# Kernel optimization log

Measured on AMD Instinct MI355X. Metric: run time of the kernel, lower is better.

Reference implementation:

```python
import jax, jax.numpy as jnp
import numpy as np

NSUB = 2          # fixed RK4 substeps per output interval (deterministic stand-in for adaptive dopri5)
SLOPE = 1.0 / 5.5  # leaky_relu negative slope used by g and OutputNN


def setup_inputs() -> dict:
    key = jax.random.key(0)
    ks = iter(jax.random.split(key, 40))
    B, Tp, Tf = 256, 32, 256
    D, H, HF, HG, HO = 1, 100, 275, 75, 75

    def rn(shape, s=0.05):
        return jax.random.normal(next(ks), shape, jnp.float32) * s

    # past: [B, Tp, 1+D] with strictly increasing times in column 0
    past_t = jnp.sort(jax.random.uniform(next(ks), (B, Tp), jnp.float32) * Tp, axis=1)
    past_x = jax.random.normal(next(ks), (B, Tp, D), jnp.float32)
    past = jnp.concatenate([past_t[:, :, None], past_x], axis=2)
    # future times start after the last past time, strictly increasing
    t_future = past_t[:, -1:] + jnp.sort(
        jax.random.uniform(next(ks), (B, Tf), jnp.float32) * 0.1 * Tf, axis=1)

    return dict(
        past=past,
        h0=jnp.zeros((B, H), jnp.float32),
        t_future=t_future,
        eps=jax.random.normal(next(ks), (H, B), jnp.float32),
        fW1=rn((HF, H + 1)), fb1=rn((HF,)), fW2=rn((HF, HF)), fb2=rn((HF,)),
        fW3=rn((H, HF)), fb3=rn((H,)),
        gru_Wih=rn((3 * H, D)), gru_Whh=rn((3 * H, H)),
        gru_bih=rn((3 * H,)), gru_bhh=rn((3 * H,)),
        gW1=rn((HG, H)), gb1=rn((HG,)), gW2=rn((HG, HG)), gb2=rn((HG,)),
        gW3=rn((2, HG)), gb3=rn((2,)),
        oW1=rn((HO, H)), ob1=rn((HO,)), oW2=rn((HO, HO)), ob2=rn((HO,)),
        oW3=rn((D, HO)), ob3=rn((D,)),
    )


def _leaky(x):
    return jnp.where(x >= 0, x, SLOPE * x)


def reference(past, h0, t_future, eps,
              fW1, fb1, fW2, fb2, fW3, fb3,
              gru_Wih, gru_Whh, gru_bih, gru_bhh,
              gW1, gb1, gW2, gb2, gW3, gb3,
              oW1, ob1, oW2, ob2, oW3, ob3):
    def field(t, y):  # t: [B], y: [B, H] -> dy/dt: [B, H]  (f module)
        x = jnp.concatenate([t[:, None], y], axis=1)
        x = jnp.tanh(x @ fW1.T + fb1)
        x = jnp.tanh(x @ fW2.T + fb2)
        return jnp.tanh(x @ fW3.T + fb3)

    def integrate(y0, t0, t1):  # batched fixed-step RK4 from t0 to t1 (per-batch times)
        dt = ((t1 - t0) / NSUB)[:, None]  # [B, 1]
        dts = dt[:, 0]
        def body(y, i):
            t = t0 + i * dts
            k1 = field(t, y)
            k2 = field(t + 0.5 * dts, y + 0.5 * dt * k1)
            k3 = field(t + 0.5 * dts, y + 0.5 * dt * k2)
            k4 = field(t + dts, y + dt * k3)
            return y + dt * (k1 + 2.0 * k2 + 2.0 * k3 + k4) / 6.0, None
        y, _ = jax.lax.scan(body, y0, jnp.arange(NSUB, dtype=y0.dtype))
        return y

    def gru(x, h):  # torch.nn.GRUCell math
        gi = x @ gru_Wih.T + gru_bih
        gh = h @ gru_Whh.T + gru_bhh
        ir, iz, inn = jnp.split(gi, 3, axis=1)
        hr, hz, hn = jnp.split(gh, 3, axis=1)
        r = jax.nn.sigmoid(ir + hr)
        z = jax.nn.sigmoid(iz + hz)
        n = jnp.tanh(inn + r * hn)
        return (1.0 - z) * n + z * h

    times = past[:, :, 0]   # [B, Tp]
    data = past[:, :, 1:]   # [B, Tp, D]

    # first GRUODE step: evolve h0 from t0-1 to t0, then GRU update with x0
    h = gru(data[:, 0], integrate(h0, times[:, 0] - 1.0, times[:, 0]))
    xs = (jnp.swapaxes(data[:, 1:], 0, 1), times[:, :-1].T, times[:, 1:].T)
    def pbody(hc, s):
        x, tp, tc = s
        return gru(x, integrate(hc, tp, tc)), None
    h, _ = jax.lax.scan(pbody, h, xs)

    # g head -> (loc, |scale|), reproducing the concat/view of the original
    gx = _leaky(h @ gW1.T + gb1)
    gx = _leaky(gx @ gW2.T + gb2)
    gx = gx @ gW3.T + gb3                                   # [B, 2]
    pr = jnp.concatenate([gx[:, 0], jnp.abs(gx[:, 1])]).reshape(-1, 2)
    loc, scale = pr[:, 0], pr[:, 1]                          # [B], [B]

    # Sampler: Normal(loc, scale).rsample([H]) reparameterized with eps [H, B]
    z0 = (loc[None, :] + scale[None, :] * eps).T             # [B, H]

    # integrate z0 across future time grid
    def fbody(y, s):
        tp, tc = s
        yn = integrate(y, tp, tc)
        return yn, yn
    _, traj = jax.lax.scan(fbody, z0, (t_future[:, :-1].T, t_future[:, 1:].T))
    out = jnp.swapaxes(jnp.concatenate([z0[None], traj], axis=0), 0, 1)  # [B, Tf, H]

    # OutputNN head
    o = _leaky(out @ oW1.T + ob1)
    o = _leaky(o @ oW2.T + ob2)
    return o @ oW3.T + ob3  # [B, Tf, D]
```

## Files before the change

### kernel.cpp

```cpp
#include <hip/hip_runtime.h>
#include <hip/hip_fp16.h>

typedef _Float16 f16;
typedef _Float16 f16x2 __attribute__((ext_vector_type(2)));
typedef _Float16 f16x8 __attribute__((ext_vector_type(8)));
typedef float f32x4 __attribute__((ext_vector_type(4)));
typedef unsigned short u16;
typedef unsigned int u32;

__device__ __forceinline__ float fdot2v(f16x2 a, f16x2 b, float c){
#if __has_builtin(__builtin_amdgcn_fdot2)
  return __builtin_amdgcn_fdot2(a, b, c, false);
#else
  return c + (float)a.x * (float)b.x + (float)a.y * (float)b.y;
#endif
}

__device__ __forceinline__ float rcp_f(float x){
#if __has_builtin(__builtin_amdgcn_rcpf)
  return __builtin_amdgcn_rcpf(x);
#else
  return 1.f / x;
#endif
}

__device__ __forceinline__ float tanh_f(float x){
  return 1.f - 2.f * rcp_f(__expf(2.f * x) + 1.f);
}
__device__ __forceinline__ float sigm_f(float x){
  return rcp_f(1.f + __expf(-x));
}
__device__ __forceinline__ float leaky_f(float x){
  return x >= 0.f ? x : x * (1.0f / 5.5f);
}

template<int NP>
__device__ __forceinline__ void ld_pairs(const float* W, int row, int ncols, int c0,
                                         f16x2* dst, bool valid){
  const float* base = W + (long)row * ncols;
#pragma unroll
  for (int p = 0; p < NP; p++){
    int c = c0 + 2 * p;
    f16x2 v;
    v.x = (valid && c     < ncols) ? (f16)base[c]     : (f16)0.f;
    v.y = (valid && c + 1 < ncols) ? (f16)base[c + 1] : (f16)0.f;
    dst[p] = v;
  }
}

template<int NCH>
__device__ __forceinline__ float dot_chunks(const f16x2* w, const f16x8* x, int chunk0){
  float a0 = 0.f, a1 = 0.f, a2 = 0.f, a3 = 0.f;
#pragma unroll
  for (int c = 0; c < NCH; c++){
    union { f16x8 v; f16x2 h[4]; } u;
    u.v = x[chunk0 + c];
    a0 = fdot2v(w[4*c + 0], u.h[0], a0);
    a1 = fdot2v(w[4*c + 1], u.h[1], a1);
    a2 = fdot2v(w[4*c + 2], u.h[2], a2);
    a3 = fdot2v(w[4*c + 3], u.h[3], a3);
  }
  return (a0 + a1) + (a2 + a3);
}

__device__ __forceinline__ f16x8 ldfrag(const float* W, int row, int ncols, int k0, bool valid){
  f16x8 v;
#pragma unroll
  for (int j = 0; j < 8; j++){
    int c = k0 + j;
    v[j] = (valid && c < ncols) ? (f16)W[(long)row * ncols + c] : (f16)0.f;
  }
  return v;
}

__device__ __forceinline__ float sel4(f32x4 a, int c){
  float v = a.x;
  v = (c == 1) ? a.y : v;
  v = (c == 2) ? a.z : v;
  v = (c == 3) ? a.w : v;
  return v;
}

#define MFMA16(A,B,C) __builtin_amdgcn_mfma_f32_16x16x32_f16((A),(B),(C),0,0,0)

struct FRM {
  f16x8 a1[2][4];
  f16x8 a2[2][9];
  f16x8 af[13];
  f16x2 w3b[9];
  float w1tw, b1w, b2w;
  float b3w;
};

struct DEC {
  f16x2 dW1[16]; f16x2 dW2[12]; f16x2 dW3;
  float ob1v, ob2v, ob3v;
};

__device__ __forceinline__ void load_field_mfma(FRM& R, int tid,
    const float* fW1, const float* fb1, const float* fW2, const float* fb2,
    const float* fW3, const float* fb3)
{
  const int lane = tid & 63, wv = tid >> 6;
  const int lm = lane & 15, lg = lane >> 4;
  const int r0 = 32 * wv + lm, r1 = r0 + 16;
#pragma unroll
  for (int c = 0; c < 4; c++){
    R.a1[0][c] = ldfrag(fW1, r0, 101, 32 * c + 8 * lg, true);
    R.a1[1][c] = ldfrag(fW1, r1, 101, 32 * c + 8 * lg, true);
  }
#pragma unroll
  for (int c = 0; c < 9; c++){
    R.a2[0][c] = ldfrag(fW2, r0, 275, 32 * c + 8 * lg, true);
    R.a2[1][c] = ldfrag(fW2, r1, 275, 32 * c + 8 * lg, true);
  }
  if (wv < 6){
    const int r3 = 16 * wv + lm;
#pragma unroll
    for (int c = 0; c < 9; c++)
      R.af[c] = ldfrag(fW3, r3, 275, 32 * c + 8 * lg, true);
#pragma unroll
    for (int c = 9; c < 13; c++) R.af[c] = (f16x8)(f16)0.f;
  } else {
    const int r2 = 256 + 16 * (wv - 6) + lm;
    const bool v2 = r2 < 275;
    const int r2c = v2 ? r2 : 0;
#pragma unroll
    for (int c = 0; c < 4; c++)
      R.af[c] = ldfrag(fW1, r2c, 101, 32 * c + 8 * lg, v2);
#pragma unroll
    for (int c = 0; c < 9; c++)
      R.af[4 + c] = ldfrag(fW2, r2c, 275, 32 * c + 8 * lg, v2);
  }
  {
    const bool w7 = (wv == 7);
    ld_pairs<9>(fW3, w7 ? (96 + lg) : 0, 275, 18 * lm, R.w3b, w7);
  }
  {
    const int s = lm >> 2;
    const bool use3 = (s == 2) && (wv >= 6);
    int rw = use3 ? (256 + 16 * (wv - 6) + 4 * lg + (lm & 3))
                  : (32 * wv + 16 * (s & 1) + 4 * lg + (lm & 3));
    int rwc = rw < 275 ? rw : 274;
    R.w1tw = fW1[rwc * 101];
    R.b1w  = fb1[rwc];
    R.b2w  = fb2[rwc];
  }
  if (wv < 6)       R.b3w = fb3[16 * wv + 4 * lg + (lm & 3)];
  else if (wv == 7) R.b3w = fb3[96 + lg];
  else              R.b3w = 0.f;
}

template<bool D>
__device__ __forceinline__ f32x4 field_eval_m(const FRM& R, const DEC& dc,
    float t, int tid, f16* ust, f16* x1s, f16* x2s,
    const f16x8* yv, f16* o1s, f16* o2s, float* outp, int tf)
{
  const int lm = tid & 15, lg = (tid >> 4) & 3, wv = tid >> 6;
  const bool x3 = (wv >= 6);
  const int nw = x3 ? 12 : 8;
  const f16x8* ub  = (const f16x8*)ust;
  const f16x8* x1b = (const f16x8*)x1s;
  const f16x8* x2b = (const f16x8*)x2s;
  const f32x4 zz = {0.f, 0.f, 0.f, 0.f};

  {
    f16x8 u0 = ub[lg], u1 = ub[4 + lg], u2 = ub[8 + lg], u3 = ub[12 + lg];
    f32x4 A0 = zz, A1 = zz, A2 = zz, B0 = zz, B1 = zz, B2 = zz;
    A0 = MFMA16(R.a1[0][0], u0, A0);  A1 = MFMA16(R.a1[1][0], u0, A1);
    B0 = MFMA16(R.a1[0][1], u1, B0);  B1 = MFMA16(R.a1[1][1], u1, B1);
    A0 = MFMA16(R.a1[0][2], u2, A0);  A1 = MFMA16(R.a1[1][2], u2, A1);
    B0 = MFMA16(R.a1[0][3], u3, B0);  B1 = MFMA16(R.a1[1][3], u3, B1);
    if (x3){
      A2 = MFMA16(R.af[0], u0, A2);  B2 = MFMA16(R.af[1], u1, B2);
      A2 = MFMA16(R.af[2], u2, A2);  B2 = MFMA16(R.af[3], u3, B2);
    }
    if (D){
      int jq = tid >> 2, qq = tid & 3;
      if (jq < 75){
        float a = dot_chunks<4>(dc.dW1, yv, 4 * qq);
        a += __shfl_xor(a, 1); a += __shfl_xor(a, 2);
        if (qq == 0) o1s[jq] = (f16)leaky_f(a + dc.ob1v);
      }
    }
    if (lm < nw){
      int s = lm >> 2, reg = lm & 3;
      int rw = (s == 2) ? (256 + 16 * (wv - 6) + 4 * lg + reg)
                        : (32 * wv + 16 * s + 4 * lg + reg);
      float v0 = sel4(A0 + B0, reg), v1 = sel4(A1 + B1, reg), v2 = sel4(A2 + B2, reg);
      float v = (s == 0) ? v0 : ((s == 1) ? v1 : v2);
      x1s[rw] = (f16)tanh_f(v + R.w1tw * t + R.b1w);
    }
  }
  __syncthreads();

  {
    f32x4 A0 = zz, A1 = zz, A2 = zz, B0 = zz, B1 = zz, B2 = zz;
#pragma unroll
    for (int c = 0; c < 5; c++){
      f16x8 bp = x1b[4 * c + lg];
      A0 = MFMA16(R.a2[0][c], bp, A0);
      A1 = MFMA16(R.a2[1][c], bp, A1);
      if (x3) A2 = MFMA16(R.af[4 + c], bp, A2);
    }
#pragma unroll
    for (int c = 5; c < 9; c++){
      f16x8 bq = x1b[4 * c + lg];
      B0 = MFMA16(R.a2[0][c], bq, B0);
      B1 = MFMA16(R.a2[1][c], bq, B1);
      if (x3) B2 = MFMA16(R.af[4 + c], bq, B2);
    }
    if (D){
      int jq = tid >> 2, qq = tid & 3;
      if (jq < 75){
        float a = dot_chunks<3>(dc.dW2, (const f16x8*)o1s, 3 * qq);
        a += __shfl_xor(a, 1); a += __shfl_xor(a, 2);
        if (qq == 0) o2s[jq] = (f16)leaky_f(a + dc.ob2v);
      }
    }
    if (lm < nw){
      int s = lm >> 2, reg = lm & 3;
      int rw = (s == 2) ? (256 + 16 * (wv - 6) + 4 * lg + reg)
                        : (32 * wv + 16 * s + 4 * lg + reg);
      float v0 = sel4(A0 + B0, reg), v1 = sel4(A1 + B1, reg), v2 = sel4(A2 + B2, reg);
      float v = (s == 0) ? v0 : ((s == 1) ? v1 : v2);
      x2s[rw] = (f16)tanh_f(v + R.b2w);
    }
  }
  __syncthreads();

  f32x4 acc3 = zz;
  if (wv < 6){
    f32x4 r0 = zz, r1 = zz;
#pragma unroll
    for (int c = 0; c < 5; c++) r0 = MFMA16(R.af[c], x2b[4 * c + lg], r0);
#pragma unroll
    for (int c = 5; c < 9; c++) r1 = MFMA16(R.af[c], x2b[4 * c + lg], r1);
    acc3 = r0 + r1;
  } else if (wv == 7){
    float a2t = 0.f;
    const f16x2* xv2 = (const f16x2*)x2s + 9 * lm;
#pragma unroll
    for (int p = 0; p < 9; p++) a2t = fdot2v(R.w3b[p], xv2[p], a2t);
    a2t += __shfl_xor(a2t, 1); a2t += __shfl_xor(a2t, 2);
    a2t += __shfl_xor(a2t, 4); a2t += __shfl_xor(a2t, 8);
    acc3.x = a2t;
  }
  if (D){
    if (wv == 6){
      int t2 = tid - 384;
      float a = 0.f;
      if (t2 < 40) a = fdot2v(dc.dW3, ((const f16x2*)o2s)[t2], 0.f);
      a += __shfl_xor(a, 1);  a += __shfl_xor(a, 2);  a += __shfl_xor(a, 4);
      a += __shfl_xor(a, 8);  a += __shfl_xor(a, 16); a += __shfl_xor(a, 32);
      if (t2 == 0) outp[tf] = a + dc.ob3v;
    }
  }
  return acc3;
}

__global__ __launch_bounds__(512, 2) void k_encode(
    const float* __restrict__ past, const float* __restrict__ h0,
    const float* __restrict__ fW1, const float* __restrict__ fb1,
    const float* __restrict__ fW2, const float* __restrict__ fb2,
    const float* __restrict__ fW3, const float* __restrict__ fb3,
    const float* __restrict__ Wih, const float* __restrict__ Whh,
    const float* __restrict__ bih, const float* __restrict__ bhh,
    const float* __restrict__ gW1, const float* __restrict__ gb1,
    const float* __restrict__ gW2, const float* __restrict__ gb2,
    const float* __restrict__ gW3, const float* __restrict__ gb3,
    float* __restrict__ gx_ws)
{
  __shared__ f16x8 ustV[16];
  __shared__ f16x8 ystV[16];
  __shared__ f16x8 x1V[36];
  __shared__ f16x8 x2V[36];
  __shared__ float yf[100];
  __shared__ float ghs[300];
  __shared__ f16x2 gW1s[75 * 52];
  __shared__ f16x2 gW2s[75 * 40];
  __shared__ f16x2 gW3s[80];
  __shared__ f16x2 g1s2[40];
  __shared__ f16x2 g2s2[40];

  const int tid = threadIdx.x;
  const int b = blockIdx.x;
  f16* ust = (f16*)ustV;
  f16* yst = (f16*)ystV;
  f16* x1s = (f16*)x1V;
  f16* x2s = (f16*)x2V;
  f16* g1s = (f16*)g1s2;
  f16* g2s = (f16*)g2s2;

  FRM R;
  load_field_mfma(R, tid, fW1, fb1, fW2, fb2, fW3, fb3);
  DEC dcz{};

  f16x2 whh[28]; float bhhv;
  f16x2 whhb[7]; float bhhbv;
  {
    int j1 = tid >> 1, h = tid & 1;
    ld_pairs<28>(Whh, j1, 100, 56 * h, whh, true);
    bhhv = bhh[j1];
    bool p2 = tid < 352;
    int j2 = 256 + (tid >> 3), s7 = tid & 7;
    ld_pairs<7>(Whh, p2 ? j2 : 0, 100, 14 * s7, whhb, p2);
    bhhbv = p2 ? bhh[j2] : 0.f;
  }
  float wihr=0,wihz=0,wihn=0,bihr=0,bihz=0,bihn=0;
  if (tid < 100){
    wihr = Wih[tid];       bihr = bih[tid];
    wihz = Wih[tid + 100]; bihz = bih[tid + 100];
    wihn = Wih[tid + 200]; bihn = bih[tid + 200];
  }
  const int jq = tid >> 2, qq = tid & 3;
  const bool lv = (qq == 0 && jq < 75);
  float gb1v = lv ? gb1[jq] : 0.f;
  float gb2v = lv ? gb2[jq] : 0.f;

  for (int i = tid; i < 75 * 52; i += 512){
    int r = i / 52, c = 2 * (i % 52);
    f16x2 v;
    v.x = (c     < 100) ? (f16)gW1[r * 100 + c]     : (f16)0.f;
    v.y = (c + 1 < 100) ? (f16)gW1[r * 100 + c + 1] : (f16)0.f;
    gW1s[i] = v;
  }
  for (int i = tid; i < 75 * 40; i += 512){
    int r = i / 40, c = 2 * (i % 40);
    f16x2 v;
    v.x = (c     < 75) ? (f16)gW2[r * 75 + c]     : (f16)0.f;
    v.y = (c + 1 < 75) ? (f16)gW2[r * 75 + c + 1] : (f16)0.f;
    gW2s[i] = v;
  }
  for (int i = tid; i < 80; i += 512){
    int r = i / 40, c = 2 * (i % 40);
    f16x2 v;
    v.x = (c     < 75) ? (f16)gW3[r * 75 + c]     : (f16)0.f;
    v.y = (c + 1 < 75) ? (f16)gW3[r * 75 + c + 1] : (f16)0.f;
    gW3s[i] = v;
  }
  for (int i = tid; i < 128; i += 512){ ust[i] = (f16)0.f; yst[i] = (f16)0.f; }
  for (int i = tid; i < 288; i += 512){ x1s[i] = (f16)0.f; x2s[i] = (f16)0.f; }
  for (int i = tid; i < 80;  i += 512){ g1s[i] = (f16)0.f; g2s[i] = (f16)0.f; }
  if (tid < 100){
    float v = h0[b * 100 + tid];
    yf[tid] = v; yst[tid] = (f16)v; ust[1 + tid] = (f16)v;
  }
  __syncthreads();

  const int lm = tid & 15, lg2 = (tid >> 4) & 3, wv = tid >> 6;
  bool wr3; int row3;
  if (wv < 6)      { wr3 = (lm < 4);  row3 = 16 * wv + 4 * lg2 + (lm & 3); }
  else if (wv == 7){ wr3 = (lm == 0); row3 = 96 + lg2; }
  else             { wr3 = false;     row3 = 0; }
  float k1v = 0.f, k2v = 0.f, k3v = 0.f;

  auto kval = [&](f32x4 a){
    float av = (wv == 7) ? a.x : sel4(a, lm);
    return tanh_f(av + R.b3w);
  };

  auto rk_interval = [&](float tp, float tc){
    float dts = (tc - tp) * 0.5f;
#pragma unroll 1
    for (int sub = 0; sub < 2; sub++){
      float t0 = tp + sub * dts;
      float yfr = 0.f;
      __syncthreads();
      if (wr3) yfr = yf[row3];
      f32x4 a = field_eval_m<false>(R, dcz, t0, tid, ust, x1s, x2s,
                                    nullptr, nullptr, nullptr, nullptr, 0);
      if (wr3){ float kv = kval(a); k1v = kv;
                ust[1 + row3] = (f16)(yfr + 0.5f * dts * kv); }
      __syncthreads();
      a = field_eval_m<false>(R, dcz, t0 + 0.5f * dts, tid, ust, x1s, x2s,
                              nullptr, nullptr, nullptr, nullptr, 0);
      if (wr3){ float kv = kval(a); k2v = kv;
                ust[1 + row3] = (f16)(yfr + 0.5f * dts * kv); }
      __syncthreads();
      a = field_eval_m<false>(R, dcz, t0 + 0.5f * dts, tid, ust, x1s, x2s,
                              nullptr, nullptr, nullptr, nullptr, 0);
      if (wr3){ float kv = kval(a); k3v = kv;
                ust[1 + row3] = (f16)(yfr + dts * kv); }
      __syncthreads();
      a = field_eval_m<false>(R, dcz, t0 + dts, tid, ust, x1s, x2s,
                              nullptr, nullptr, nullptr, nullptr, 0);
      if (wr3){
        float kv = kval(a);
        float yn = yfr + dts * (k1v + 2.f * (k2v + k3v) + kv) * (1.f / 6.f);
        yf[row3] = yn; ust[1 + row3] = (f16)yn; yst[row3] = (f16)yn;
      }
    }
  };

  const float* prow = past + b * 64;
#pragma unroll 1
  for (int st = 0; st < 32; st++){
    float tc = prow[2 * st];
    float tp = (st == 0) ? (tc - 1.f) : prow[2 * st - 2];
    rk_interval(tp, tc);
    __syncthreads();
    {
      int j1 = tid >> 1, h = tid & 1;
      float a = dot_chunks<7>(whh, ystV, 7 * h);
      a += __shfl_xor(a, 1);
      if (!h) ghs[j1] = a + bhhv;
      if (tid < 352){
        int s7 = tid & 7;
        float a2 = 0.f;
        const f16x2* yv2 = (const f16x2*)ystV + 7 * s7;
#pragma unroll
        for (int p = 0; p < 7; p++) a2 = fdot2v(whhb[p], yv2[p], a2);
        a2 += __shfl_xor(a2, 1); a2 += __shfl_xor(a2, 2); a2 += __shfl_xor(a2, 4);
        if (s7 == 0) ghs[256 + (tid >> 3)] = a2 + bhhbv;
      }
    }
    __syncthreads();
    if (tid < 100){
      float x = prow[2 * st + 1];
      float r = sigm_f(x * wihr + bihr + ghs[tid]);
      float z = sigm_f(x * wihz + bihz + ghs[tid + 100]);
      float n = tanh_f(x * wihn + bihn + r * ghs[tid + 200]);
      float hn = (1.f - z) * n + z * yf[tid];
      yf[tid] = hn; yst[tid] = (f16)hn; ust[1 + tid] = (f16)hn;
    }
  }

  __syncthreads();
  {
    float a = 0.f;
    const f16x2* yv = (const f16x2*)ystV + 13 * qq;
    if (jq < 75){
#pragma unroll
      for (int p = 0; p < 13; p++) a = fdot2v(gW1s[jq * 52 + 13 * qq + p], yv[p], a);
    }
    a += __shfl_xor(a, 1); a += __shfl_xor(a, 2);
    if (lv) g1s[jq] = (f16)leaky_f(a + gb1v);
  }
  __syncthreads();
  {
    float a = 0.f;
    const f16x2* xv = (const f16x2*)g1s + 10 * qq;
    if (jq < 75){
#pragma unroll
      for (int p = 0; p < 10; p++) a = fdot2v(gW2s[jq * 40 + 10 * qq + p], xv[p], a);
    }
    a += __shfl_xor(a, 1); a += __shfl_xor(a, 2);
    if (lv) g2s[jq] = (f16)leaky_f(a + gb2v);
  }
  __syncthreads();
  if (tid < 2){
    const f16x2* g2v = (const f16x2*)g2s;
    float a = gb3[tid];
    for (int p = 0; p < 40; p++) a = fdot2v(gW3s[tid * 40 + p], g2v[p], a);
    gx_ws[b * 2 + tid] = a;
  }
}

__global__ __launch_bounds__(512, 2) void k_forecast(
    const float* __restrict__ t_future, const float* __restrict__ eps,
    const float* __restrict__ fW1, const float* __restrict__ fb1,
    const float* __restrict__ fW2, const float* __restrict__ fb2,
    const float* __restrict__ fW3, const float* __restrict__ fb3,
    const float* __restrict__ oW1, const float* __restrict__ ob1,
    const float* __restrict__ oW2, const float* __restrict__ ob2,
    const float* __restrict__ oW3, const float* __restrict__ ob3,
    const float* __restrict__ gx_ws, float* __restrict__ out)
{
  __shared__ f16x8 ustV[16];
  __shared__ f16x8 ystV[16];
  __shared__ f16x8 x1V[36];
  __shared__ f16x8 x2V[36];
  __shared__ f16x8 o1V[12];
  __shared__ f16x8 o2V[12];

  const int tid = threadIdx.x;
  const int b = blockIdx.x;
  f16* ust = (f16*)ustV;
  f16* yst = (f16*)ystV;
  f16* x1s = (f16*)x1V;
  f16* x2s = (f16*)x2V;
  f16* o1s = (f16*)o1V;
  f16* o2s = (f16*)o2V;
  float* outb = out + b * 256;

  FRM R;
  load_field_mfma(R, tid, fW1, fb1, fW2, fb2, fW3, fb3);

  const int jq = tid >> 2, qq = tid & 3;
  const bool dv = jq < 75;
  const bool lv = (qq == 0 && dv);
  DEC dc;
  ld_pairs<16>(oW1, dv ? jq : 0, 100, 32 * qq, dc.dW1, dv);
  ld_pairs<12>(oW2, dv ? jq : 0, 75, 24 * qq, dc.dW2, dv);
  {
    int t2 = tid - 384;
    bool v = (t2 >= 0 && t2 < 40);
    ld_pairs<1>(oW3, 0, 75, v ? 2 * t2 : 0, &dc.dW3, v);
  }
  dc.ob1v = lv ? ob1[jq] : 0.f;
  dc.ob2v = lv ? ob2[jq] : 0.f;
  dc.ob3v = ob3[0];

  for (int i = tid; i < 128; i += 512){ ust[i] = (f16)0.f; yst[i] = (f16)0.f; }
  for (int i = tid; i < 288; i += 512){ x1s[i] = (f16)0.f; x2s[i] = (f16)0.f; }
  for (int i = tid; i < 96;  i += 512){ o1s[i] = (f16)0.f; o2s[i] = (f16)0.f; }

  const int lm = tid & 15, lg2 = (tid >> 4) & 3, wv = tid >> 6;
  bool wr3; int row3;
  if (wv < 6)      { wr3 = (lm < 4);  row3 = 16 * wv + 4 * lg2 + (lm & 3); }
  else if (wv == 7){ wr3 = (lm == 0); row3 = 96 + lg2; }
  else             { wr3 = false;     row3 = 0; }
  float k1v = 0.f, k2v = 0.f, k3v = 0.f, yfr = 0.f;

  auto kval = [&](f32x4 a){
    float av = (wv == 7) ? a.x : sel4(a, lm);
    return tanh_f(av + R.b3w);
  };

  if (wr3){
    float loc, scl;
    if (b < 128){ loc = gx_ws[4 * b];              scl = gx_ws[4 * b + 2]; }
    else        { loc = fabsf(gx_ws[4 * b - 511]); scl = fabsf(gx_ws[4 * b - 509]); }
    float e = eps[row3 * 256 + b];
    yfr = loc + scl * e;
    yst[row3] = (f16)yfr; ust[1 + row3] = (f16)yfr;
  }
  __syncthreads();

  const float* trow = t_future + b * 256;
#pragma unroll 1
  for (int iv = 0; iv < 255; iv++){
    float tp = trow[iv];
    float tc = trow[iv + 1];
    float dts = (tc - tp) * 0.5f;
#pragma unroll 1
    for (int sub = 0; sub < 2; sub++){
      float t0 = tp + sub * dts;
      __syncthreads();
      f32x4 a;
      if (sub == 0)
        a = field_eval_m<true >(R, dc, t0, tid, ust, x1s, x2s,
                                (const f16x8*)yst, o1s, o2s, outb, iv);
      else
        a = field_eval_m<false>(R, dc, t0, tid, ust, x1s, x2s,
                                nullptr, nullptr, nullptr, nullptr, 0);
      if (wr3){ float kv = kval(a); k1v = kv;
                ust[1 + row3] = (f16)(yfr + 0.5f * dts * kv); }
      __syncthreads();
      a = field_eval_m<false>(R, dc, t0 + 0.5f * dts, tid, ust, x1s, x2s,
                              nullptr, nullptr, nullptr, nullptr, 0);
      if (wr3){ float kv = kval(a); k2v = kv;
                ust[1 + row3] = (f16)(yfr + 0.5f * dts * kv); }
      __syncthreads();
      a = field_eval_m<false>(R, dc, t0 + 0.5f * dts, tid, ust, x1s, x2s,
                              nullptr, nullptr, nullptr, nullptr, 0);
      if (wr3){ float kv = kval(a); k3v = kv;
                ust[1 + row3] = (f16)(yfr + dts * kv); }
      __syncthreads();
      a = field_eval_m<false>(R, dc, t0 + dts, tid, ust, x1s, x2s,
                              nullptr, nullptr, nullptr, nullptr, 0);
      if (wr3){
        float kv = kval(a);
        float yn = yfr + dts * (k1v + 2.f * (k2v + k3v) + kv) * (1.f / 6.f);
        yfr = yn; ust[1 + row3] = (f16)yn; yst[row3] = (f16)yn;
      }
    }
  }

  __syncthreads();
  if (dv){
    float a = dot_chunks<4>(dc.dW1, (const f16x8*)yst, 4 * qq);
    a += __shfl_xor(a, 1); a += __shfl_xor(a, 2);
    if (qq == 0) o1s[jq] = (f16)leaky_f(a + dc.ob1v);
  }
  __syncthreads();
  if (dv){
    float a = dot_chunks<3>(dc.dW2, (const f16x8*)o1s, 3 * qq);
    a += __shfl_xor(a, 1); a += __shfl_xor(a, 2);
    if (qq == 0) o2s[jq] = (f16)leaky_f(a + dc.ob2v);
  }
  __syncthreads();
  if (wv == 6){
    int t2 = tid - 384;
    float a = 0.f;
    if (t2 < 40) a = fdot2v(dc.dW3, ((const f16x2*)o2s)[t2], 0.f);
    a += __shfl_xor(a, 1);  a += __shfl_xor(a, 2);  a += __shfl_xor(a, 4);
    a += __shfl_xor(a, 8);  a += __shfl_xor(a, 16); a += __shfl_xor(a, 32);
    if (t2 == 0) outb[255] = a + dc.ob3v;
  }
}

extern "C" void kernel_launch(void* const* d_in, const int* in_sizes, int n_in,
                              void* d_out, int out_size, void* d_ws, size_t ws_size,
                              hipStream_t stream) {
  (void)in_sizes; (void)n_in; (void)out_size; (void)ws_size;
  const float* past     = (const float*)d_in[0];
  const float* h0       = (const float*)d_in[1];
  const float* t_future = (const float*)d_in[2];
  const float* eps      = (const float*)d_in[3];
  const float* fW1 = (const float*)d_in[4];  const float* fb1 = (const float*)d_in[5];
  const float* fW2 = (const float*)d_in[6];  const float* fb2 = (const float*)d_in[7];
  const float* fW3 = (const float*)d_in[8];  const float* fb3 = (const float*)d_in[9];
  const float* Wih = (const float*)d_in[10]; const float* Whh = (const float*)d_in[11];
  const float* bih = (const float*)d_in[12]; const float* bhh = (const float*)d_in[13];
  const float* gW1 = (const float*)d_in[14]; const float* gb1 = (const float*)d_in[15];
  const float* gW2 = (const float*)d_in[16]; const float* gb2 = (const float*)d_in[17];
  const float* gW3 = (const float*)d_in[18]; const float* gb3 = (const float*)d_in[19];
  const float* oW1 = (const float*)d_in[20]; const float* ob1 = (const float*)d_in[21];
  const float* oW2 = (const float*)d_in[22]; const float* ob2 = (const float*)d_in[23];
  const float* oW3 = (const float*)d_in[24]; const float* ob3 = (const float*)d_in[25];
  float* gxws = (float*)d_ws;
  float* out = (float*)d_out;

  hipLaunchKernelGGL(k_encode, dim3(256), dim3(512), 0, stream,
      past, h0, fW1, fb1, fW2, fb2, fW3, fb3,
      Wih, Whh, bih, bhh, gW1, gb1, gW2, gb2, gW3, gb3, gxws);
  hipLaunchKernelGGL(k_forecast, dim3(256), dim3(512), 0, stream,
      t_future, eps, fW1, fb1, fW2, fb2, fW3, fb3,
      oW1, ob1, oW2, ob2, oW3, ob3, gxws, out);
}
```

Before: 3.489 ms.

## Double block size to 16 waves and redistribute field MLP rows across waves

Both kernels now launch 1024 threads per block instead of 512. Each wave owns one 16-row MFMA tile of the first two layers rather than two. The tail rows 256-274 move to fdot2 reductions in waves 0-4, and fW3 moves to waves 10-15. Decoder weights now share register space with the tail/fW3 fragments through a union, and the GRU hidden matmul reads Whh from shared memory with one thread per row instead of register-held pairs. The intent is to shorten the per-step serial critical path and cut register pressure, at the cost of more threads synchronising at each barrier, extra LDS for Whh, and some idle waves.

```diff
diff --git a/kernel.cpp b/kernel.cpp
--- a/kernel.cpp
+++ b/kernel.cpp
@@ -5,8 +5,6 @@
 typedef _Float16 f16x2 __attribute__((ext_vector_type(2)));
 typedef _Float16 f16x8 __attribute__((ext_vector_type(8)));
 typedef float f32x4 __attribute__((ext_vector_type(4)));
-typedef unsigned short u16;
-typedef unsigned int u32;
 
 __device__ __forceinline__ float fdot2v(f16x2 a, f16x2 b, float c){
 #if __has_builtin(__builtin_amdgcn_fdot2)
@@ -83,18 +81,17 @@
 
 #define MFMA16(A,B,C) __builtin_amdgcn_mfma_f32_16x16x32_f16((A),(B),(C),0,0,0)
 
+union AF {
+  f16x8 v8[9];
+  f16x2 v2[36];
+};
 struct FRM {
-  f16x8 a1[2][4];
-  f16x8 a2[2][9];
-  f16x8 af[13];
-  f16x2 w3b[9];
+  f16x8 a1[4];
+  f16x8 a2[9];
+  AF af;
+  float c0, c1, c2;
   float w1tw, b1w, b2w;
   float b3w;
-};
-
-struct DEC {
-  f16x2 dW1[16]; f16x2 dW2[12]; f16x2 dW3;
-  float ob1v, ob2v, ob3v;
 };
 
 __device__ __forceinline__ void load_field_mfma(FRM& R, int tid,
@@ -103,163 +100,146 @@
 {
   const int lane = tid & 63, wv = tid >> 6;
   const int lm = lane & 15, lg = lane >> 4;
-  const int r0 = 32 * wv + lm, r1 = r0 + 16;
-#pragma unroll
-  for (int c = 0; c < 4; c++){
-    R.a1[0][c] = ldfrag(fW1, r0, 101, 32 * c + 8 * lg, true);
-    R.a1[1][c] = ldfrag(fW1, r1, 101, 32 * c + 8 * lg, true);
-  }
-#pragma unroll
-  for (int c = 0; c < 9; c++){
-    R.a2[0][c] = ldfrag(fW2, r0, 275, 32 * c + 8 * lg, true);
-    R.a2[1][c] = ldfrag(fW2, r1, 275, 32 * c + 8 * lg, true);
-  }
-  if (wv < 6){
-    const int r3 = 16 * wv + lm;
+  const int r0 = 16 * wv + lm;
+#pragma unroll
+  for (int c = 0; c < 4; c++)
+    R.a1[c] = ldfrag(fW1, r0, 101, 32 * c + 8 * lg, true);
+#pragma unroll
+  for (int c = 0; c < 9; c++)
+    R.a2[c] = ldfrag(fW2, r0, 275, 32 * c + 8 * lg, true);
+
+#pragma unroll
+  for (int c = 0; c < 9; c++) R.af.v8[c] = (f16x8)(f16)0.f;
+  R.c0 = 0.f; R.c1 = 0.f; R.c2 = 0.f;
+
+  if (wv >= 10){
+    const int r3 = 16 * (wv - 10) + lm;
 #pragma unroll
     for (int c = 0; c < 9; c++)
-      R.af[c] = ldfrag(fW3, r3, 275, 32 * c + 8 * lg, true);
-#pragma unroll
-    for (int c = 9; c < 13; c++) R.af[c] = (f16x8)(f16)0.f;
-  } else {
-    const int r2 = 256 + 16 * (wv - 6) + lm;
-    const bool v2 = r2 < 275;
-    const int r2c = v2 ? r2 : 0;
-#pragma unroll
-    for (int c = 0; c < 4; c++)
-      R.af[c] = ldfrag(fW1, r2c, 101, 32 * c + 8 * lg, v2);
-#pragma unroll
-    for (int c = 0; c < 9; c++)
-      R.af[4 + c] = ldfrag(fW2, r2c, 275, 32 * c + 8 * lg, v2);
+      R.af.v8[c] = ldfrag(fW3, r3, 275, 32 * c + 8 * lg, true);
+  } else if (wv < 5){
+    const bool p2 = tid < 304;
+    const int m = tid >> 4, s = tid & 15;
+    const int j2 = 256 + (p2 ? m : 0);
+    ld_pairs<4>(fW1, j2, 101, 8 * s, R.af.v2 + 0, p2);
+    ld_pairs<9>(fW2, j2, 275, 18 * s, R.af.v2 + 4, p2);
+    R.c0 = (p2 && s == 0) ? fW1[j2 * 101] : 0.f;
+    R.c1 = p2 ? fb1[j2] : 0.f;
+    R.c2 = p2 ? fb2[j2] : 0.f;
+    if (wv == 4)
+      ld_pairs<9>(fW3, 96 + lg, 275, 18 * lm, R.af.v2 + 13, true);
   }
   {
-    const bool w7 = (wv == 7);
-    ld_pairs<9>(fW3, w7 ? (96 + lg) : 0, 275, 18 * lm, R.w3b, w7);
-  }
-  {
-    const int s = lm >> 2;
-    const bool use3 = (s == 2) && (wv >= 6);
-    int rw = use3 ? (256 + 16 * (wv - 6) + 4 * lg + (lm & 3))
-                  : (32 * wv + 16 * (s & 1) + 4 * lg + (lm & 3));
-    int rwc = rw < 275 ? rw : 274;
+    int rwc = 16 * wv + 4 * lg + (lm & 3);
     R.w1tw = fW1[rwc * 101];
     R.b1w  = fb1[rwc];
     R.b2w  = fb2[rwc];
   }
-  if (wv < 6)       R.b3w = fb3[16 * wv + 4 * lg + (lm & 3)];
-  else if (wv == 7) R.b3w = fb3[96 + lg];
+  if (wv >= 10)     R.b3w = fb3[16 * (wv - 10) + 4 * lg + (lm & 3)];
+  else if (wv == 4) R.b3w = fb3[96 + lg];
   else              R.b3w = 0.f;
 }
 
 template<bool D>
-__device__ __forceinline__ f32x4 field_eval_m(const FRM& R, const DEC& dc,
+__device__ __forceinline__ f32x4 field_eval_m(const FRM& R,
     float t, int tid, f16* ust, f16* x1s, f16* x2s,
     const f16x8* yv, f16* o1s, f16* o2s, float* outp, int tf)
 {
   const int lm = tid & 15, lg = (tid >> 4) & 3, wv = tid >> 6;
-  const bool x3 = (wv >= 6);
-  const int nw = x3 ? 12 : 8;
   const f16x8* ub  = (const f16x8*)ust;
   const f16x8* x1b = (const f16x8*)x1s;
   const f16x8* x2b = (const f16x8*)x2s;
   const f32x4 zz = {0.f, 0.f, 0.f, 0.f};
+  const bool tailw = tid < 304;
+  const int dj = (tid - 320) >> 2, dq = tid & 3;
+  const bool decw = D && (tid >= 320) && (dj < 75);
 
   {
-    f16x8 u0 = ub[lg], u1 = ub[4 + lg], u2 = ub[8 + lg], u3 = ub[12 + lg];
-    f32x4 A0 = zz, A1 = zz, A2 = zz, B0 = zz, B1 = zz, B2 = zz;
-    A0 = MFMA16(R.a1[0][0], u0, A0);  A1 = MFMA16(R.a1[1][0], u0, A1);
-    B0 = MFMA16(R.a1[0][1], u1, B0);  B1 = MFMA16(R.a1[1][1], u1, B1);
-    A0 = MFMA16(R.a1[0][2], u2, A0);  A1 = MFMA16(R.a1[1][2], u2, A1);
-    B0 = MFMA16(R.a1[0][3], u3, B0);  B1 = MFMA16(R.a1[1][3], u3, B1);
-    if (x3){
-      A2 = MFMA16(R.af[0], u0, A2);  B2 = MFMA16(R.af[1], u1, B2);
-      A2 = MFMA16(R.af[2], u2, A2);  B2 = MFMA16(R.af[3], u3, B2);
-    }
-    if (D){
-      int jq = tid >> 2, qq = tid & 3;
-      if (jq < 75){
-        float a = dot_chunks<4>(dc.dW1, yv, 4 * qq);
-        a += __shfl_xor(a, 1); a += __shfl_xor(a, 2);
-        if (qq == 0) o1s[jq] = (f16)leaky_f(a + dc.ob1v);
-      }
-    }
-    if (lm < nw){
-      int s = lm >> 2, reg = lm & 3;
-      int rw = (s == 2) ? (256 + 16 * (wv - 6) + 4 * lg + reg)
-                        : (32 * wv + 16 * s + 4 * lg + reg);
-      float v0 = sel4(A0 + B0, reg), v1 = sel4(A1 + B1, reg), v2 = sel4(A2 + B2, reg);
-      float v = (s == 0) ? v0 : ((s == 1) ? v1 : v2);
-      x1s[rw] = (f16)tanh_f(v + R.w1tw * t + R.b1w);
-    }
+    f32x4 A = zz, B = zz;
+    A = MFMA16(R.a1[0], ub[lg],      A);
+    B = MFMA16(R.a1[1], ub[4 + lg],  B);
+    A = MFMA16(R.a1[2], ub[8 + lg],  A);
+    B = MFMA16(R.a1[3], ub[12 + lg], B);
+    if (tailw){
+      int s = tid & 15;
+      float a2 = (s == 0) ? R.c0 * t : 0.f;
+      const f16x2* uv2 = (const f16x2*)ust + 4 * s;
+      const f16x2* w1b = R.af.v2;
+#pragma unroll
+      for (int p = 0; p < 4; p++) a2 = fdot2v(w1b[p], uv2[p], a2);
+      a2 += __shfl_xor(a2, 1); a2 += __shfl_xor(a2, 2);
+      a2 += __shfl_xor(a2, 4); a2 += __shfl_xor(a2, 8);
+      if (s == 0) x1s[256 + (tid >> 4)] = (f16)tanh_f(a2 + R.c1);
+    }
+    if (decw){
+      float a = dot_chunks<4>(R.af.v2, yv, 4 * dq);
+      a += __shfl_xor(a, 1); a += __shfl_xor(a, 2);
+      if (dq == 0) o1s[dj] = (f16)leaky_f(a + R.c0);
+    }
+    f32x4 acc = A + B;
+    if (lm < 4)
+      x1s[16 * wv + 4 * lg + lm] = (f16)tanh_f(sel4(acc, lm) + R.w1tw * t + R.b1w);
   }
   __syncthreads();
 
   {
-    f32x4 A0 = zz, A1 = zz, A2 = zz, B0 = zz, B1 = zz, B2 = zz;
-#pragma unroll
-    for (int c = 0; c < 5; c++){
-      f16x8 bp = x1b[4 * c + lg];
-      A0 = MFMA16(R.a2[0][c], bp, A0);
-      A1 = MFMA16(R.a2[1][c], bp, A1);
-      if (x3) A2 = MFMA16(R.af[4 + c], bp, A2);
-    }
-#pragma unroll
-    for (int c = 5; c < 9; c++){
-      f16x8 bq = x1b[4 * c + lg];
-      B0 = MFMA16(R.a2[0][c], bq, B0);
-      B1 = MFMA16(R.a2[1][c], bq, B1);
-      if (x3) B2 = MFMA16(R.af[4 + c], bq, B2);
-    }
-    if (D){
-      int jq = tid >> 2, qq = tid & 3;
-      if (jq < 75){
-        float a = dot_chunks<3>(dc.dW2, (const f16x8*)o1s, 3 * qq);
-        a += __shfl_xor(a, 1); a += __shfl_xor(a, 2);
-        if (qq == 0) o2s[jq] = (f16)leaky_f(a + dc.ob2v);
-      }
-    }
-    if (lm < nw){
-      int s = lm >> 2, reg = lm & 3;
-      int rw = (s == 2) ? (256 + 16 * (wv - 6) + 4 * lg + reg)
-                        : (32 * wv + 16 * s + 4 * lg + reg);
-      float v0 = sel4(A0 + B0, reg), v1 = sel4(A1 + B1, reg), v2 = sel4(A2 + B2, reg);
-      float v = (s == 0) ? v0 : ((s == 1) ? v1 : v2);
-      x2s[rw] = (f16)tanh_f(v + R.b2w);
-    }
+    f32x4 A = zz, B = zz;
+#pragma unroll
+    for (int c = 0; c < 5; c++) A = MFMA16(R.a2[c], x1b[4 * c + lg], A);
+#pragma unroll
+    for (int c = 5; c < 9; c++) B = MFMA16(R.a2[c], x1b[4 * c + lg], B);
+    if (tailw){
+      int s = tid & 15;
+      float a2 = 0.f;
+      const f16x2* xv2 = (const f16x2*)x1s + 9 * s;
+      const f16x2* w2b = R.af.v2 + 4;
+#pragma unroll
+      for (int p = 0; p < 9; p++) a2 = fdot2v(w2b[p], xv2[p], a2);
+      a2 += __shfl_xor(a2, 1); a2 += __shfl_xor(a2, 2);
+      a2 += __shfl_xor(a2, 4); a2 += __shfl_xor(a2, 8);
+      if (s == 0) x2s[256 + (tid >> 4)] = (f16)tanh_f(a2 + R.c2);
+    }
+    if (decw){
+      float a = dot_chunks<3>(R.af.v2 + 16, (const f16x8*)o1s, 3 * dq);
+      a += __shfl_xor(a, 1); a += __shfl_xor(a, 2);
+      if (dq == 0) o2s[dj] = (f16)leaky_f(a + R.c1);
+    }
+    f32x4 acc = A + B;
+    if (lm < 4)
+      x2s[16 * wv + 4 * lg + lm] = (f16)tanh_f(sel4(acc, lm) + R.b2w);
   }
   __syncthreads();
 
   f32x4 acc3 = zz;
-  if (wv < 6){
+  if (wv >= 10){
     f32x4 r0 = zz, r1 = zz;
 #pragma unroll
-    for (int c = 0; c < 5; c++) r0 = MFMA16(R.af[c], x2b[4 * c + lg], r0);
-#pragma unroll
-    for (int c = 5; c < 9; c++) r1 = MFMA16(R.af[c], x2b[4 * c + lg], r1);
+    for (int c = 0; c < 5; c++) r0 = MFMA16(R.af.v8[c], x2b[4 * c + lg], r0);
+#pragma unroll
+    for (int c = 5; c < 9; c++) r1 = MFMA16(R.af.v8[c], x2b[4 * c + lg], r1);
     acc3 = r0 + r1;
-  } else if (wv == 7){
-    float a2t = 0.f;
+  } else if (wv == 4){
+    float a2 = 0.f;
     const f16x2* xv2 = (const f16x2*)x2s + 9 * lm;
-#pragma unroll
-    for (int p = 0; p < 9; p++) a2t = fdot2v(R.w3b[p], xv2[p], a2t);
-    a2t += __shfl_xor(a2t, 1); a2t += __shfl_xor(a2t, 2);
-    a2t += __shfl_xor(a2t, 4); a2t += __shfl_xor(a2t, 8);
-    acc3.x = a2t;
-  }
-  if (D){
-    if (wv == 6){
-      int t2 = tid - 384;
-      float a = 0.f;
-      if (t2 < 40) a = fdot2v(dc.dW3, ((const f16x2*)o2s)[t2], 0.f);
-      a += __shfl_xor(a, 1);  a += __shfl_xor(a, 2);  a += __shfl_xor(a, 4);
-      a += __shfl_xor(a, 8);  a += __shfl_xor(a, 16); a += __shfl_xor(a, 32);
-      if (t2 == 0) outp[tf] = a + dc.ob3v;
-    }
+    const f16x2* w3b = R.af.v2 + 13;
+#pragma unroll
+    for (int p = 0; p < 9; p++) a2 = fdot2v(w3b[p], xv2[p], a2);
+    a2 += __shfl_xor(a2, 1); a2 += __shfl_xor(a2, 2);
+    a2 += __shfl_xor(a2, 4); a2 += __shfl_xor(a2, 8);
+    acc3.x = a2;
+  }
+  if (D && wv == 6){
+    int t2 = tid - 384;
+    float a = 0.f;
+    if (t2 < 40) a = fdot2v(R.af.v2[28], ((const f16x2*)o2s)[t2], 0.f);
+    a += __shfl_xor(a, 1);  a += __shfl_xor(a, 2);  a += __shfl_xor(a, 4);
+    a += __shfl_xor(a, 8);  a += __shfl_xor(a, 16); a += __shfl_xor(a, 32);
+    if (t2 == 0) outp[tf] = a + R.c2;
   }
   return acc3;
 }
 
-__global__ __launch_bounds__(512, 2) void k_encode(
+__global__ __launch_bounds__(1024, 4) void k_encode(
     const float* __restrict__ past, const float* __restrict__ h0,
     const float* __restrict__ fW1, const float* __restrict__ fb1,
     const float* __restrict__ fW2, const float* __restrict__ fb2,
@@ -277,6 +257,7 @@
   __shared__ f16x8 x2V[36];
   __shared__ float yf[100];
   __shared__ float ghs[300];
+  __shared__ f16x2 whh_lds[300 * 53];
   __shared__ f16x2 gW1s[75 * 52];
   __shared__ f16x2 gW2s[75 * 40];
   __shared__ f16x2 gW3s[80];
@@ -294,54 +275,51 @@
 
   FRM R;
   load_field_mfma(R, tid, fW1, fb1, fW2, fb2, fW3, fb3);
-  DEC dcz{};
-
-  f16x2 whh[28]; float bhhv;
-  f16x2 whhb[7]; float bhhbv;
-  {
-    int j1 = tid >> 1, h = tid & 1;
-    ld_pairs<28>(Whh, j1, 100, 56 * h, whh, true);
-    bhhv = bhh[j1];
-    bool p2 = tid < 352;
-    int j2 = 256 + (tid >> 3), s7 = tid & 7;
-    ld_pairs<7>(Whh, p2 ? j2 : 0, 100, 14 * s7, whhb, p2);
-    bhhbv = p2 ? bhh[j2] : 0.f;
-  }
+
   float wihr=0,wihz=0,wihn=0,bihr=0,bihz=0,bihn=0;
   if (tid < 100){
     wihr = Wih[tid];       bihr = bih[tid];
     wihz = Wih[tid + 100]; bihz = bih[tid + 100];
     wihn = Wih[tid + 200]; bihn = bih[tid + 200];
   }
+  float bhhj = (tid < 300) ? bhh[tid] : 0.f;
+
   const int jq = tid >> 2, qq = tid & 3;
   const bool lv = (qq == 0 && jq < 75);
   float gb1v = lv ? gb1[jq] : 0.f;
   float gb2v = lv ? gb2[jq] : 0.f;
 
-  for (int i = tid; i < 75 * 52; i += 512){
+  for (int i = tid; i < 300 * 53; i += 1024){
+    int r = i / 53, c = 2 * (i % 53);
+    f16x2 v;
+    v.x = (c     < 100) ? (f16)Whh[r * 100 + c]     : (f16)0.f;
+    v.y = (c + 1 < 100) ? (f16)Whh[r * 100 + c + 1] : (f16)0.f;
+    whh_lds[i] = v;
+  }
+  for (int i = tid; i < 75 * 52; i += 1024){
     int r = i / 52, c = 2 * (i % 52);
     f16x2 v;
     v.x = (c     < 100) ? (f16)gW1[r * 100 + c]     : (f16)0.f;
     v.y = (c + 1 < 100) ? (f16)gW1[r * 100 + c + 1] : (f16)0.f;
     gW1s[i] = v;
   }
-  for (int i = tid; i < 75 * 40; i += 512){
+  for (int i = tid; i < 75 * 40; i += 1024){
     int r = i / 40, c = 2 * (i % 40);
     f16x2 v;
     v.x = (c     < 75) ? (f16)gW2[r * 75 + c]     : (f16)0.f;
     v.y = (c + 1 < 75) ? (f16)gW2[r * 75 + c + 1] : (f16)0.f;
     gW2s[i] = v;
   }
-  for (int i = tid; i < 80; i += 512){
+  for (int i = tid; i < 80; i += 1024){
     int r = i / 40, c = 2 * (i % 40);
     f16x2 v;
     v.x = (c     < 75) ? (f16)gW3[r * 75 + c]     : (f16)0.f;
     v.y = (c + 1 < 75) ? (f16)gW3[r * 75 + c + 1] : (f16)0.f;
     gW3s[i] = v;
   }
-  for (int i = tid; i < 128; i += 512){ ust[i] = (f16)0.f; yst[i] = (f16)0.f; }
-  for (int i = tid; i < 288; i += 512){ x1s[i] = (f16)0.f; x2s[i] = (f16)0.f; }
-  for (int i = tid; i < 80;  i += 512){ g1s[i] = (f16)0.f; g2s[i] = (f16)0.f; }
+  for (int i = tid; i < 128; i += 1024){ ust[i] = (f16)0.f; yst[i] = (f16)0.f; }
+  for (int i = tid; i < 288; i += 1024){ x1s[i] = (f16)0.f; x2s[i] = (f16)0.f; }
+  for (int i = tid; i < 80;  i += 1024){ g1s[i] = (f16)0.f; g2s[i] = (f16)0.f; }
   if (tid < 100){
     float v = h0[b * 100 + tid];
     yf[tid] = v; yst[tid] = (f16)v; ust[1 + tid] = (f16)v;
@@ -350,13 +328,13 @@
 
   const int lm = tid & 15, lg2 = (tid >> 4) & 3, wv = tid >> 6;
   bool wr3; int row3;
-  if (wv < 6)      { wr3 = (lm < 4);  row3 = 16 * wv + 4 * lg2 + (lm & 3); }
-  else if (wv == 7){ wr3 = (lm == 0); row3 = 96 + lg2; }
+  if (wv >= 10)    { wr3 = (lm < 4);  row3 = 16 * (wv - 10) + 4 * lg2 + (lm & 3); }
+  else if (wv == 4){ wr3 = (lm == 0); row3 = 96 + lg2; }
   else             { wr3 = false;     row3 = 0; }
   float k1v = 0.f, k2v = 0.f, k3v = 0.f;
 
   auto kval = [&](f32x4 a){
-    float av = (wv == 7) ? a.x : sel4(a, lm);
+    float av = (wv == 4) ? a.x : sel4(a, lm);
     return tanh_f(av + R.b3w);
   };
 
@@ -368,22 +346,22 @@
       float yfr = 0.f;
       __syncthreads();
       if (wr3) yfr = yf[row3];
-      f32x4 a = field_eval_m<false>(R, dcz, t0, tid, ust, x1s, x2s,
+      f32x4 a = field_eval_m<false>(R, t0, tid, ust, x1s, x2s,
                                     nullptr, nullptr, nullptr, nullptr, 0);
       if (wr3){ float kv = kval(a); k1v = kv;
                 ust[1 + row3] = (f16)(yfr + 0.5f * dts * kv); }
       __syncthreads();
-      a = field_eval_m<false>(R, dcz, t0 + 0.5f * dts, tid, ust, x1s, x2s,
+      a = field_eval_m<false>(R, t0 + 0.5f * dts, tid, ust, x1s, x2s,
                               nullptr, nullptr, nullptr, nullptr, 0);
       if (wr3){ float kv = kval(a); k2v = kv;
                 ust[1 + row3] = (f16)(yfr + 0.5f * dts * kv); }
       __syncthreads();
-      a = field_eval_m<false>(R, dcz, t0 + 0.5f * dts, tid, ust, x1s, x2s,
+      a = field_eval_m<false>(R, t0 + 0.5f * dts, tid, ust, x1s, x2s,
                               nullptr, nullptr, nullptr, nullptr, 0);
       if (wr3){ float kv = kval(a); k3v = kv;
                 ust[1 + row3] = (f16)(yfr + dts * kv); }
       __syncthreads();
-      a = field_eval_m<false>(R, dcz, t0 + dts, tid, ust, x1s, x2s,
+      a = field_eval_m<false>(R, t0 + dts, tid, ust, x1s, x2s,
                               nullptr, nullptr, nullptr, nullptr, 0);
       if (wr3){
         float kv = kval(a);
@@ -400,20 +378,20 @@
     float tp = (st == 0) ? (tc - 1.f) : prow[2 * st - 2];
     rk_interval(tp, tc);
     __syncthreads();
-    {
-      int j1 = tid >> 1, h = tid & 1;
-      float a = dot_chunks<7>(whh, ystV, 7 * h);
-      a += __shfl_xor(a, 1);
-      if (!h) ghs[j1] = a + bhhv;
-      if (tid < 352){
-        int s7 = tid & 7;
-        float a2 = 0.f;
-        const f16x2* yv2 = (const f16x2*)ystV + 7 * s7;
-#pragma unroll
-        for (int p = 0; p < 7; p++) a2 = fdot2v(whhb[p], yv2[p], a2);
-        a2 += __shfl_xor(a2, 1); a2 += __shfl_xor(a2, 2); a2 += __shfl_xor(a2, 4);
-        if (s7 == 0) ghs[256 + (tid >> 3)] = a2 + bhhbv;
+    if (tid < 300){
+      const f16x2* wrow = whh_lds + tid * 53;
+      const f16x2* yv2 = (const f16x2*)ystV;
+      float a0 = 0.f, a1 = 0.f, a2 = 0.f, a3 = 0.f;
+#pragma unroll
+      for (int p = 0; p < 48; p += 4){
+        a0 = fdot2v(wrow[p],     yv2[p],     a0);
+        a1 = fdot2v(wrow[p + 1], yv2[p + 1], a1);
+        a2 = fdot2v(wrow[p + 2], yv2[p + 2], a2);
+        a3 = fdot2v(wrow[p + 3], yv2[p + 3], a3);
       }
+      a0 = fdot2v(wrow[48], yv2[48], a0);
+      a1 = fdot2v(wrow[49], yv2[49], a1);
+      ghs[tid] = (a0 + a1) + (a2 + a3) + bhhj;
     }
     __syncthreads();
     if (tid < 100){
@@ -457,7 +435,7 @@
   }
 }
 
-__global__ __launch_bounds__(512, 2) void k_forecast(
+__global__ __launch_bounds__(1024, 4) void k_forecast(
     const float* __restrict__ t_future, const float* __restrict__ eps,
     const float* __restrict__ fW1, const float* __restrict__ fb1,
     const float* __restrict__ fW2, const float* __restrict__ fb2,
@@ -487,34 +465,37 @@
   FRM R;
   load_field_mfma(R, tid, fW1, fb1, fW2, fb2, fW3, fb3);
 
-  const int jq = tid >> 2, qq = tid & 3;
-  const bool dv = jq < 75;
-  const bool lv = (qq == 0 && dv);
-  DEC dc;
-  ld_pairs<16>(oW1, dv ? jq : 0, 100, 32 * qq, dc.dW1, dv);
-  ld_pairs<12>(oW2, dv ? jq : 0, 75, 24 * qq, dc.dW2, dv);
-  {
-    int t2 = tid - 384;
-    bool v = (t2 >= 0 && t2 < 40);
-    ld_pairs<1>(oW3, 0, 75, v ? 2 * t2 : 0, &dc.dW3, v);
-  }
-  dc.ob1v = lv ? ob1[jq] : 0.f;
-  dc.ob2v = lv ? ob2[jq] : 0.f;
-  dc.ob3v = ob3[0];
-
-  for (int i = tid; i < 128; i += 512){ ust[i] = (f16)0.f; yst[i] = (f16)0.f; }
-  for (int i = tid; i < 288; i += 512){ x1s[i] = (f16)0.f; x2s[i] = (f16)0.f; }
-  for (int i = tid; i < 96;  i += 512){ o1s[i] = (f16)0.f; o2s[i] = (f16)0.f; }
-
-  const int lm = tid & 15, lg2 = (tid >> 4) & 3, wv = tid >> 6;
+  const int wv = tid >> 6;
+  const int dj = (tid - 320) >> 2, dq = tid & 3;
+  const bool dvv = (tid >= 320) && (dj < 75);
+  if (wv >= 5 && wv <= 9){
+    int jd = dvv ? dj : 0;
+    ld_pairs<16>(oW1, jd, 100, 32 * dq, R.af.v2 + 0,  dvv);
+    ld_pairs<12>(oW2, jd, 75,  24 * dq, R.af.v2 + 16, dvv);
+    R.c0 = dvv ? ob1[jd] : 0.f;
+    R.c1 = dvv ? ob2[jd] : 0.f;
+    R.c2 = 0.f;
+    if (wv == 6){
+      int t2 = tid - 384;
+      bool v = t2 < 40;
+      ld_pairs<1>(oW3, 0, 75, v ? 2 * t2 : 0, R.af.v2 + 28, v);
+      R.c2 = ob3[0];
+    }
+  }
+
+  for (int i = tid; i < 128; i += 1024){ ust[i] = (f16)0.f; yst[i] = (f16)0.f; }
+  for (int i = tid; i < 288; i += 1024){ x1s[i] = (f16)0.f; x2s[i] = (f16)0.f; }
+  for (int i = tid; i < 96;  i += 1024){ o1s[i] = (f16)0.f; o2s[i] = (f16)0.f; }
+
+  const int lm = tid & 15, lg2 = (tid >> 4) & 3;
   bool wr3; int row3;
-  if (wv < 6)      { wr3 = (lm < 4);  row3 = 16 * wv + 4 * lg2 + (lm & 3); }
-  else if (wv == 7){ wr3 = (lm == 0); row3 = 96 + lg2; }
+  if (wv >= 10)    { wr3 = (lm < 4);  row3 = 16 * (wv - 10) + 4 * lg2 + (lm & 3); }
+  else if (wv == 4){ wr3 = (lm == 0); row3 = 96 + lg2; }
   else             { wr3 = false;     row3 = 0; }
   float k1v = 0.f, k2v = 0.f, k3v = 0.f, yfr = 0.f;
 
   auto kval = [&](f32x4 a){
-    float av = (wv == 7) ? a.x : sel4(a, lm);
+    float av = (wv == 4) ? a.x : sel4(a, lm);
     return tanh_f(av + R.b3w);
   };
 
@@ -540,25 +521,25 @@
       __syncthreads();
       f32x4 a;
       if (sub == 0)
-        a = field_eval_m<true >(R, dc, t0, tid, ust, x1s, x2s,
+        a = field_eval_m<true >(R, t0, tid, ust, x1s, x2s,
                                 (const f16x8*)yst, o1s, o2s, outb, iv);
       else
-        a = field_eval_m<false>(R, dc, t0, tid, ust, x1s, x2s,
+        a = field_eval_m<false>(R, t0, tid, ust, x1s, x2s,
                                 nullptr, nullptr, nullptr, nullptr, 0);
       if (wr3){ float kv = kval(a); k1v = kv;
                 ust[1 + row3] = (f16)(yfr + 0.5f * dts * kv); }
       __syncthreads();
-      a = field_eval_m<false>(R, dc, t0 + 0.5f * dts, tid, ust, x1s, x2s,
+      a = field_eval_m<false>(R, t0 + 0.5f * dts, tid, ust, x1s, x2s,
                               nullptr, nullptr, nullptr, nullptr, 0);
       if (wr3){ float kv = kval(a); k2v = kv;
                 ust[1 + row3] = (f16)(yfr + 0.5f * dts * kv); }
       __syncthreads();
-      a = field_eval_m<false>(R, dc, t0 + 0.5f * dts, tid, ust, x1s, x2s,
+      a = field_eval_m<false>(R, t0 + 0.5f * dts, tid, ust, x1s, x2s,
                               nullptr, nullptr, nullptr, nullptr, 0);
       if (wr3){ float kv = kval(a); k3v = kv;
                 ust[1 + row3] = (f16)(yfr + dts * kv); }
       __syncthreads();
-      a = field_eval_m<false>(R, dc, t0 + dts, tid, ust, x1s, x2s,
+      a = field_eval_m<false>(R, t0 + dts, tid, ust, x1s, x2s,
                               nullptr, nullptr, nullptr, nullptr, 0);
       if (wr3){
         float kv = kval(a);
@@ -569,25 +550,25 @@
   }
 
   __syncthreads();
-  if (dv){
-    float a = dot_chunks<4>(dc.dW1, (const f16x8*)yst, 4 * qq);
+  if (dvv){
+    float a = dot_chunks<4>(R.af.v2, (const f16x8*)yst, 4 * dq);
     a += __shfl_xor(a, 1); a += __shfl_xor(a, 2);
-    if (qq == 0) o1s[jq] = (f16)leaky_f(a + dc.ob1v);
-  }
-  __syncthreads();
-  if (dv){
-    float a = dot_chunks<3>(dc.dW2, (const f16x8*)o1s, 3 * qq);
+    if (dq == 0) o1s[dj] = (f16)leaky_f(a + R.c0);
+  }
+  __syncthreads();
+  if (dvv){
+    float a = dot_chunks<3>(R.af.v2 + 16, (const f16x8*)o1s, 3 * dq);
     a += __shfl_xor(a, 1); a += __shfl_xor(a, 2);
-    if (qq == 0) o2s[jq] = (f16)leaky_f(a + dc.ob2v);
+    if (dq == 0) o2s[dj] = (f16)leaky_f(a + R.c1);
   }
   __syncthreads();
   if (wv == 6){
     int t2 = tid - 384;
     float a = 0.f;
-    if (t2 < 40) a = fdot2v(dc.dW3, ((const f16x2*)o2s)[t2], 0.f);
+    if (t2 < 40) a = fdot2v(R.af.v2[28], ((const f16x2*)o2s)[t2], 0.f);
     a += __shfl_xor(a, 1);  a += __shfl_xor(a, 2);  a += __shfl_xor(a, 4);
     a += __shfl_xor(a, 8);  a += __shfl_xor(a, 16); a += __shfl_xor(a, 32);
-    if (t2 == 0) outb[255] = a + dc.ob3v;
+    if (t2 == 0) outb[255] = a + R.c2;
   }
 }
 
@@ -613,10 +594,10 @@
   float* gxws = (float*)d_ws;
   float* out = (float*)d_out;
 
-  hipLaunchKernelGGL(k_encode, dim3(256), dim3(512), 0, stream,
+  hipLaunchKernelGGL(k_encode, dim3(256), dim3(1024), 0, stream,
       past, h0, fW1, fb1, fW2, fb2, fW3, fb3,
       Wih, Whh, bih, bhh, gW1, gb1, gW2, gb2, gW3, gb3, gxws);
-  hipLaunchKernelGGL(k_forecast, dim3(256), dim3(512), 0, stream,
+  hipLaunchKernelGGL(k_forecast, dim3(256), dim3(1024), 0, stream,
       t_future, eps, fW1, fb1, fW2, fb2, fW3, fb3,
       oW1, ob1, oW2, ob2, oW3, ob3, gxws, out);
 }
```

Result: slower. 5.330 ms (+52.8%).
